# Kernel tuning notes

Measured on AMD Instinct MI355X. Metric: run time of the kernel, lower is better.

## Reference

```python
import jax, jax.numpy as jnp
import numpy as np

N = 100000
E = 1600000
IN, HID, OUT = 128, 256, 128


def setup_inputs() -> dict:
    key = jax.random.key(0)
    ks = jax.random.split(key, 8)
    x = jax.random.normal(ks[0], (N, IN), dtype=jnp.float32)
    edge_index = jax.random.randint(ks[1], (2, E), 0, N, dtype=jnp.int64)
    # PyG SAGEConv params: lin_l (neighbor aggr, with bias), lin_r (root, no bias)
    def glorot(k, shape):
        fan_in = shape[1]
        return jax.random.normal(k, shape, dtype=jnp.float32) / jnp.sqrt(jnp.float32(fan_in))
    W1l = glorot(ks[2], (HID, IN)); b1 = jnp.zeros((HID,), jnp.float32)
    W1r = glorot(ks[3], (HID, IN))
    W2l = glorot(ks[4], (OUT, HID)); b2 = jnp.zeros((OUT,), jnp.float32)
    W2r = glorot(ks[5], (OUT, HID))
    return {"x": x, "edge_index": edge_index, "W1l": W1l, "b1": b1,
            "W1r": W1r, "W2l": W2l, "b2": b2, "W2r": W2r}


def sage_conv(x, row, col, Wl, b, Wr, n_nodes):
    # mean-aggregate neighbor features x[row] at target nodes col
    msg = x[row]                                               # [E, d]
    s = jax.ops.segment_sum(msg, col, num_segments=n_nodes)    # [N, d]
    deg = jax.ops.segment_sum(jnp.ones((row.shape[0], 1), x.dtype), col,
                              num_segments=n_nodes)            # [N, 1]
    mean = s / jnp.maximum(deg, 1.0)
    return mean @ Wl.T + b + x @ Wr.T


def reference(x, edge_index, W1l, b1, W1r, W2l, b2, W2r):
    row, col = edge_index[0], edge_index[1]
    h = sage_conv(x, row, col, W1l, b1, W1r, N)
    h = jax.nn.relu(h)
    # dropout is identity in eval mode
    out = sage_conv(h, row, col, W2l, b2, W2r, N)
    return out
```

## Files before the change

kernel.cpp:

```cpp
#include <hip/hip_runtime.h>
#include <hip/hip_bf16.h>
#include <hip/hip_fp16.h>

#define NN 100000
#define NE 1600000
#define NCHUNK ((NN + 127) / 128)
#define NPB 512
#define NB 256
#define CHUNK 8192
#define NCH ((NE + CHUNK - 1) / CHUNK)

typedef __attribute__((ext_vector_type(8))) short short8;
typedef __attribute__((ext_vector_type(4))) float float4v;
typedef __attribute__((ext_vector_type(2))) float float2v;

__device__ __forceinline__ unsigned short f2bf(float f) {
    unsigned int b = __float_as_uint(f);
    return (unsigned short)((b + 0x7fffu + ((b >> 16) & 1u)) >> 16);
}
__device__ __forceinline__ unsigned int pack_bf16(float lo, float hi) {
    return (unsigned int)f2bf(lo) | ((unsigned int)f2bf(hi) << 16);
}
__device__ __forceinline__ void addp8(float* a, uint2 u) {
    float2v f;
    f = __builtin_amdgcn_cvt_pk_f32_fp8(u.x, false); a[0] += f.x; a[1] += f.y;
    f = __builtin_amdgcn_cvt_pk_f32_fp8(u.x, true);  a[2] += f.x; a[3] += f.y;
    f = __builtin_amdgcn_cvt_pk_f32_fp8(u.y, false); a[4] += f.x; a[5] += f.y;
    f = __builtin_amdgcn_cvt_pk_f32_fp8(u.y, true);  a[6] += f.x; a[7] += f.y;
}
__device__ __forceinline__ unsigned char f2fp8(float v) {
    int r = __builtin_amdgcn_cvt_pk_fp8_f32(v, v, 0, false);
    return (unsigned char)(r & 0xff);
}
__device__ __forceinline__ unsigned short pack2fp8(float lo, float hi) {
    int r = __builtin_amdgcn_cvt_pk_fp8_f32(lo, hi, 0, false);
    return (unsigned short)(r & 0xffff);
}
__device__ __forceinline__ float h2f(unsigned short u) {
    return __half2float(__ushort_as_half(u));
}

__global__ void k_prep(const float* x, const float* W1l, const float* W1r,
                       const float* W2l, const float* W2r, const int* ei,
                       unsigned int* axb_u, unsigned short* xf8, unsigned short* wb1,
                       unsigned short* wb2, int* bcnt) {
    __shared__ int hh[NB];
    int b = blockIdx.x, t = threadIdx.x;
    if (b < 25000) {
        int tt = b * 256 + t;
        int node = tt >> 6, i = tt & 63;
        float2 v = ((const float2*)x)[tt];
        axb_u[(size_t)node * 128 + 64 + i] = pack_bf16(v.x, v.y);
        xf8[(size_t)node * 64 + i] = pack2fp8(v.x, v.y);
    } else if (b < 25128) {
        int i = (b - 25000) * 256 + t;
        int r1 = i >> 7, c1 = i & 127;
        wb1[r1 * 256 + c1]       = f2bf(W1l[i]);
        wb1[r1 * 256 + 128 + c1] = f2bf(W1r[i]);
        wb2[i]         = f2bf(W2l[i]);
        wb2[32768 + i] = f2bf(W2r[i]);
    } else {
        hh[t] = 0;
        __syncthreads();
        int e0 = (b - 25128) * 6250;
        for (int e = e0 + t; e < e0 + 6250; e += 256)
            atomicAdd(&hh[ei[NE + e] >> 9], 1);
        __syncthreads();
        if (hh[t]) atomicAdd(&bcnt[t], hh[t]);
    }
}

__global__ void k_bscan(const int* bcnt, int* boff, int* bcur) {
    __shared__ int s[NB];
    int t = threadIdx.x;
    int v = bcnt[t];
    s[t] = v;
    __syncthreads();
    for (int d = 1; d < NB; d <<= 1) {
        int val = (t >= d) ? s[t - d] : 0;
        __syncthreads();
        s[t] += val;
        __syncthreads();
    }
    boff[t + 1] = s[t];
    if (t == 0) boff[0] = 0;
    bcur[t] = s[t] - v;
}

__global__ __launch_bounds__(256) void k_bscatter(const int* ei, int* bcur, unsigned int* pairs) {
    __shared__ unsigned int buf[CHUNK];
    __shared__ int cnt[NB];
    __shared__ int lbase[NB];
    __shared__ int lcur[NB];
    __shared__ int gpos[NB];
    int t = threadIdx.x;
    int e0 = blockIdx.x * CHUNK;
    int nedge = NE - e0; if (nedge > CHUNK) nedge = CHUNK;
    cnt[t] = 0;
    __syncthreads();
    for (int i = t; i < nedge; i += 256)
        atomicAdd(&cnt[ei[NE + e0 + i] >> 9], 1);
    __syncthreads();
    int v = cnt[t];
    lcur[t] = v;
    __syncthreads();
    for (int d = 1; d < NB; d <<= 1) {
        int val = (t >= d) ? lcur[t - d] : 0;
        __syncthreads();
        lcur[t] += val;
        __syncthreads();
    }
    lbase[t] = lcur[t] - v;
    gpos[t] = atomicAdd(&bcur[t], v);
    __syncthreads();
    lcur[t] = lbase[t];
    __syncthreads();
    for (int i = t; i < nedge; i += 256) {
        int r = ei[e0 + i], c = ei[NE + e0 + i];
        int b = c >> 9;
        int p = atomicAdd(&lcur[b], 1);
        buf[p] = (unsigned)r | ((unsigned)(c & 511) << 17);
    }
    __syncthreads();
    int wv = t >> 6, lane = t & 63;
    for (int b = wv; b < NB; b += 4) {
        int n = cnt[b], lb = lbase[b], gp = gpos[b];
        for (int i = lane; i < n; i += 64)
            pairs[gp + i] = buf[lb + i];
    }
}

__global__ __launch_bounds__(256) void k_build(const unsigned int* pairs, const int* boff,
                                               int* off, int* deg, int* csr) {
    __shared__ int ldeg[NPB];
    __shared__ int lcur[NPB];
    __shared__ int sscan[256];
    int b = blockIdx.x;
    int nbase = b * NPB;
    if (nbase >= NN) return;
    int t = threadIdx.x;
    int base = boff[b], cntb = boff[b + 1] - base;
    ldeg[t] = 0; ldeg[t + 256] = 0;
    __syncthreads();
    for (int i = t; i < cntb; i += 256) {
        unsigned int pr = pairs[base + i];
        atomicAdd(&ldeg[pr >> 17], 1);
    }
    __syncthreads();
    int d0 = ldeg[2 * t], d1 = ldeg[2 * t + 1];
    int v = d0 + d1;
    sscan[t] = v;
    __syncthreads();
    for (int d = 1; d < 256; d <<= 1) {
        int val = (t >= d) ? sscan[t - d] : 0;
        __syncthreads();
        sscan[t] += val;
        __syncthreads();
    }
    int ex = sscan[t] - v;
    lcur[2 * t] = ex; lcur[2 * t + 1] = ex + d0;
    __syncthreads();
    int nloc = NN - nbase; if (nloc > NPB) nloc = NPB;
    for (int ln = t; ln < nloc; ln += 256) {
        off[nbase + ln] = base + lcur[ln];
        deg[nbase + ln] = ldeg[ln];
    }
    __syncthreads();
    for (int i = t; i < cntb; i += 256) {
        unsigned int pr = pairs[base + i];
        int p = atomicAdd(&lcur[pr >> 17], 1);
        csr[base + p] = (int)(pr & 0x1FFFFu);
    }
}

__global__ void k_agg1(const uint2* xf8, const int* off, const int* deg,
                       const int* csr, unsigned int* axb_w) {
    int wid = (blockIdx.x * 256 + threadIdx.x) >> 6;
    if (wid >= NN) return;
    int lane = threadIdx.x & 63;
    int sub = lane >> 4, l16 = lane & 15;
    int start = off[wid], d = deg[wid];
    const uint2* gp = xf8 + l16;
    float a[8] = {0.f, 0.f, 0.f, 0.f, 0.f, 0.f, 0.f, 0.f};
    int j = sub;
    for (; j + 4 < d; j += 8) {
        int n0 = csr[start + j];
        int n1 = csr[start + j + 4];
        uint2 u0 = gp[(size_t)n0 * 16];
        uint2 u1 = gp[(size_t)n1 * 16];
        addp8(a, u0); addp8(a, u1);
    }
    if (j < d) {
        int nb = csr[start + j];
        uint2 u = gp[(size_t)nb * 16];
        addp8(a, u);
    }
#pragma unroll
    for (int i = 0; i < 8; i++) {
        a[i] += __shfl_xor(a[i], 16, 64);
        a[i] += __shfl_xor(a[i], 32, 64);
    }
    if (sub == 0) {
        float inv = 1.0f / (float)(d > 0 ? d : 1);
        uint4 o;
        o.x = pack_bf16(a[0] * inv, a[1] * inv);
        o.y = pack_bf16(a[2] * inv, a[3] * inv);
        o.z = pack_bf16(a[4] * inv, a[5] * inv);
        o.w = pack_bf16(a[6] * inv, a[7] * inv);
        *(uint4*)(axb_w + (size_t)wid * 128 + (l16 << 2)) = o;
    }
}

__global__ void k_agg2(const uint2* g, const int* off, const int* deg,
                       const int* csr, const unsigned short* partial, float* out) {
    int wid = (blockIdx.x * 256 + threadIdx.x) >> 6;
    if (wid >= NN) return;
    int lane = threadIdx.x & 63;
    int sub = lane >> 4, l16 = lane & 15;
    int start = off[wid], d = deg[wid];
    const uint2* gp = g + l16;
    float a[8] = {0.f, 0.f, 0.f, 0.f, 0.f, 0.f, 0.f, 0.f};
    int j = sub;
    for (; j + 4 < d; j += 8) {
        int n0 = csr[start + j];
        int n1 = csr[start + j + 4];
        uint2 u0 = gp[(size_t)n0 * 16];
        uint2 u1 = gp[(size_t)n1 * 16];
        addp8(a, u0); addp8(a, u1);
    }
    if (j < d) {
        int nb = csr[start + j];
        uint2 u = gp[(size_t)nb * 16];
        addp8(a, u);
    }
#pragma unroll
    for (int i = 0; i < 8; i++) {
        a[i] += __shfl_xor(a[i], 16, 64);
        a[i] += __shfl_xor(a[i], 32, 64);
    }
    if (sub == 0) {
        float inv = 1.0f / (float)(d > 0 ? d : 1);
        uint4 pu = *(const uint4*)(partial + (size_t)wid * 128 + (l16 << 3));
        float4 c0, c1;
        c0.x = h2f(pu.x & 0xffff) + a[0] * inv; c0.y = h2f(pu.x >> 16) + a[1] * inv;
        c0.z = h2f(pu.y & 0xffff) + a[2] * inv; c0.w = h2f(pu.y >> 16) + a[3] * inv;
        c1.x = h2f(pu.z & 0xffff) + a[4] * inv; c1.y = h2f(pu.z >> 16) + a[5] * inv;
        c1.z = h2f(pu.w & 0xffff) + a[6] * inv; c1.w = h2f(pu.w >> 16) + a[7] * inv;
        float4* po = (float4*)(out + (size_t)wid * 128) + (l16 << 1);
        po[0] = c0; po[1] = c1;
    }
}

#define BROW 264
__global__ __launch_bounds__(256, 4) void k_gemm1(const unsigned short* A, const unsigned short* wb,
                                                  const float* b1, unsigned short* H) {
    __shared__ unsigned short Bs[64 * BROW];
    int t = threadIdx.x;
    int cg = blockIdx.x & 3, chunk = blockIdx.x >> 2;
    {
        const short8* src = (const short8*)(wb + (size_t)cg * 64 * 256);
        short8* dst = (short8*)Bs;
#pragma unroll
        for (int i = 0; i < 8; i++) {
            int gi = i * 256 + t;
            int r = gi >> 5, c = gi & 31;
            dst[r * 33 + c] = src[gi];
        }
    }
    __syncthreads();
    int wv = t >> 6, lane = t & 63;
    int mrow = lane & 15, quad = lane >> 4;
    int base = chunk * 128 + wv * 32;
    if (base >= NN) return;
    float bias[4];
#pragma unroll
    for (int ctl = 0; ctl < 4; ctl++) bias[ctl] = b1[cg * 64 + ctl * 16 + mrow];
    float4v acc[2][4];
#pragma unroll
    for (int h = 0; h < 2; h++)
#pragma unroll
        for (int ctl = 0; ctl < 4; ctl++) acc[h][ctl] = (float4v)(0.0f);
    const short8* a0p = (const short8*)(A + (size_t)(base + mrow) * 256);
    const short8* a1p = (const short8*)(A + (size_t)(base + 16 + mrow) * 256);
#pragma unroll
    for (int kk = 0; kk < 8; kk++) {
        short8 a0 = a0p[kk * 4 + quad];
        short8 a1 = a1p[kk * 4 + quad];
        int koff = kk * 32 + quad * 8;
#pragma unroll
        for (int ctl = 0; ctl < 4; ctl++) {
            short8 b = *(const short8*)(Bs + (ctl * 16 + mrow) * BROW + koff);
            acc[0][ctl] = __builtin_amdgcn_mfma_f32_16x16x32_bf16(a0, b, acc[0][ctl], 0, 0, 0);
            acc[1][ctl] = __builtin_amdgcn_mfma_f32_16x16x32_bf16(a1, b, acc[1][ctl], 0, 0, 0);
        }
    }
#pragma unroll
    for (int ctl = 0; ctl < 4; ctl++) {
        int col = cg * 64 + ctl * 16 + mrow;
#pragma unroll
        for (int h = 0; h < 2; h++)
#pragma unroll
            for (int r = 0; r < 4; r++) {
                int node = base + h * 16 + quad * 4 + r;
                float v = acc[h][ctl][r] + bias[ctl];
                H[(size_t)node * 256 + col] = f2bf(fmaxf(v, 0.f));
            }
    }
}

__global__ __launch_bounds__(256, 4) void k_gemm2(const unsigned short* A, const unsigned short* wb,
                                                  const float* b2, unsigned char* g,
                                                  unsigned short* partial) {
    __shared__ unsigned short Bs[64 * BROW];
    int t = threadIdx.x;
    int cg = blockIdx.x & 3, chunk = blockIdx.x >> 2;
    {
        const short8* src = (const short8*)(wb + (size_t)cg * 64 * 256);
        short8* dst = (short8*)Bs;
#pragma unroll
        for (int i = 0; i < 8; i++) {
            int gi = i * 256 + t;
            int r = gi >> 5, c = gi & 31;
            dst[r * 33 + c] = src[gi];
        }
    }
    __syncthreads();
    int wv = t >> 6, lane = t & 63;
    int mrow = lane & 15, quad = lane >> 4;
    int base = chunk * 128 + wv * 32;
    if (base >= NN) return;
    float bias[4];
#pragma unroll
    for (int ctl = 0; ctl < 4; ctl++)
        bias[ctl] = (cg >= 2) ? b2[cg * 64 + ctl * 16 + mrow - 128] : 0.f;
    float4v acc[2][4];
#pragma unroll
    for (int h = 0; h < 2; h++)
#pragma unroll
        for (int ctl = 0; ctl < 4; ctl++) acc[h][ctl] = (float4v)(0.0f);
    const short8* a0p = (const short8*)(A + (size_t)(base + mrow) * 256);
    const short8* a1p = (const short8*)(A + (size_t)(base + 16 + mrow) * 256);
#pragma unroll
    for (int kk = 0; kk < 8; kk++) {
        short8 a0 = a0p[kk * 4 + quad];
        short8 a1 = a1p[kk * 4 + quad];
        int koff = kk * 32 + quad * 8;
#pragma unroll
        for (int ctl = 0; ctl < 4; ctl++) {
            short8 b = *(const short8*)(Bs + (ctl * 16 + mrow) * BROW + koff);
            acc[0][ctl] = __builtin_amdgcn_mfma_f32_16x16x32_bf16(a0, b, acc[0][ctl], 0, 0, 0);
            acc[1][ctl] = __builtin_amdgcn_mfma_f32_16x16x32_bf16(a1, b, acc[1][ctl], 0, 0, 0);
        }
    }
    if (cg < 2) {
#pragma unroll
        for (int ctl = 0; ctl < 4; ctl++) {
            int col = cg * 64 + ctl * 16 + mrow;
#pragma unroll
            for (int h = 0; h < 2; h++)
#pragma unroll
                for (int r = 0; r < 4; r++) {
                    int node = base + h * 16 + quad * 4 + r;
                    g[(size_t)node * 128 + col] = f2fp8(acc[h][ctl][r]);
                }
        }
    } else {
#pragma unroll
        for (int ctl = 0; ctl < 4; ctl++) {
            int pcol = cg * 64 + ctl * 16 + mrow - 128;
#pragma unroll
            for (int h = 0; h < 2; h++)
#pragma unroll
                for (int r = 0; r < 4; r++) {
                    int node = base + h * 16 + quad * 4 + r;
                    __half hf = __float2half(acc[h][ctl][r] + bias[ctl]);
                    partial[(size_t)node * 128 + pcol] = __half_as_ushort(hf);
                }
        }
    }
}

extern "C" void kernel_launch(void* const* d_in, const int* in_sizes, int n_in,
                              void* d_out, int out_size, void* d_ws, size_t ws_size,
                              hipStream_t stream) {
    const float* x   = (const float*)d_in[0];
    const int*   ei  = (const int*)d_in[1];
    const float* W1l = (const float*)d_in[2];
    const float* b1  = (const float*)d_in[3];
    const float* W1r = (const float*)d_in[4];
    const float* W2l = (const float*)d_in[5];
    const float* b2  = (const float*)d_in[6];
    const float* W2r = (const float*)d_in[7];
    float* out = (float*)d_out;

    char* p = (char*)d_ws;
    unsigned int* axb = (unsigned int*)p; p += (size_t)NN * 256 * 2;
    unsigned short* h = (unsigned short*)p; p += (size_t)NN * 256 * 2;
    unsigned char* g  = (unsigned char*)p; p += (size_t)NN * 128;
    unsigned short* xf8 = (unsigned short*)p; p += (size_t)NN * 128;
    unsigned short* wb1 = (unsigned short*)p; p += 65536 * 2;
    unsigned short* wb2 = (unsigned short*)p; p += 65536 * 2;
    int* deg  = (int*)p; p += (size_t)NN * 4;
    int* off  = (int*)p; p += (size_t)NN * 4;
    int* csr  = (int*)p; p += (size_t)NE * 4;
    int* bcnt = (int*)p; p += NB * 4;
    int* boff = (int*)p; p += (NB + 1) * 4;
    int* bcur = (int*)p; p += NB * 4;
    if (ws_size < (size_t)(p - (char*)d_ws)) return;
    unsigned int* pairs = (unsigned int*)h;
    unsigned short* partial = (unsigned short*)axb;

    hipMemsetAsync(bcnt, 0, NB * 4, stream);
    k_prep<<<25384, 256, 0, stream>>>(x, W1l, W1r, W2l, W2r, ei, axb, xf8, wb1, wb2, bcnt);
    k_bscan<<<1, NB, 0, stream>>>(bcnt, boff, bcur);
    k_bscatter<<<NCH, 256, 0, stream>>>(ei, bcur, pairs);
    k_build<<<NB, 256, 0, stream>>>(pairs, boff, off, deg, csr);
    k_agg1<<<NN * 64 / 256, 256, 0, stream>>>((const uint2*)xf8, off, deg, csr, axb);
    k_gemm1<<<NCHUNK * 4, 256, 0, stream>>>((const unsigned short*)axb, wb1, b1, h);
    k_gemm2<<<NCHUNK * 4, 256, 0, stream>>>(h, wb2, b2, g, partial);
    k_agg2<<<25000, 256, 0, stream>>>((const uint2*)g, off, deg, csr, partial, out);
}
```

Before: 373.3 us.

## Add padded 16-neighbor index table, grid-stride prep, swizzled GEMM grid, larger agg blocks

Builds a fixed-width table holding the first 16 neighbor indices of each node. The aggregation kernels load it with one coalesced read per lane and broadcast it with shuffles, avoiding serial CSR index loads for low-degree nodes. It also makes the prep kernel process 8 elements per thread with fewer blocks, reorders GEMM block indices so the 4 column groups of 8 chunks run together for better L2 reuse of A, uses 512-thread blocks in the aggregation kernels, and hoists the partial load in agg2 ahead of the gather loop. In exchange it adds extra workspace and writes in the CSR build, and the table is used only if the workspace is large enough.

```diff
diff --git a/kernel.cpp b/kernel.cpp
--- a/kernel.cpp
+++ b/kernel.cpp
@@ -46,14 +46,17 @@
                        unsigned short* wb2, int* bcnt) {
     __shared__ int hh[NB];
     int b = blockIdx.x, t = threadIdx.x;
-    if (b < 25000) {
-        int tt = b * 256 + t;
-        int node = tt >> 6, i = tt & 63;
-        float2 v = ((const float2*)x)[tt];
-        axb_u[(size_t)node * 128 + 64 + i] = pack_bf16(v.x, v.y);
-        xf8[(size_t)node * 64 + i] = pack2fp8(v.x, v.y);
-    } else if (b < 25128) {
-        int i = (b - 25000) * 256 + t;
+    if (b < 3125) {
+#pragma unroll
+        for (int k = 0; k < 8; k++) {
+            int tt = b * 2048 + k * 256 + t;
+            int node = tt >> 6, i = tt & 63;
+            float2 v = ((const float2*)x)[tt];
+            axb_u[(size_t)node * 128 + 64 + i] = pack_bf16(v.x, v.y);
+            xf8[(size_t)node * 64 + i] = pack2fp8(v.x, v.y);
+        }
+    } else if (b < 3253) {
+        int i = (b - 3125) * 256 + t;
         int r1 = i >> 7, c1 = i & 127;
         wb1[r1 * 256 + c1]       = f2bf(W1l[i]);
         wb1[r1 * 256 + 128 + c1] = f2bf(W1r[i]);
@@ -62,7 +65,7 @@
     } else {
         hh[t] = 0;
         __syncthreads();
-        int e0 = (b - 25128) * 6250;
+        int e0 = (b - 3253) * 6250;
         for (int e = e0 + t; e < e0 + 6250; e += 256)
             atomicAdd(&hh[ei[NE + e] >> 9], 1);
         __syncthreads();
@@ -131,9 +134,10 @@
 }
 
 __global__ __launch_bounds__(256) void k_build(const unsigned int* pairs, const int* boff,
-                                               int* off, int* deg, int* csr) {
+                                               int* off, int* deg, int* csr, int* csr16) {
     __shared__ int ldeg[NPB];
     __shared__ int lcur[NPB];
+    __shared__ int lini[NPB];
     __shared__ int sscan[256];
     int b = blockIdx.x;
     int nbase = b * NPB;
@@ -158,7 +162,8 @@
         __syncthreads();
     }
     int ex = sscan[t] - v;
-    lcur[2 * t] = ex; lcur[2 * t + 1] = ex + d0;
+    lcur[2 * t] = ex;      lcur[2 * t + 1] = ex + d0;
+    lini[2 * t] = ex;      lini[2 * t + 1] = ex + d0;
     __syncthreads();
     int nloc = NN - nbase; if (nloc > NPB) nloc = NPB;
     for (int ln = t; ln < nloc; ln += 256) {
@@ -166,23 +171,50 @@
         deg[nbase + ln] = ldeg[ln];
     }
     __syncthreads();
-    for (int i = t; i < cntb; i += 256) {
-        unsigned int pr = pairs[base + i];
-        int p = atomicAdd(&lcur[pr >> 17], 1);
-        csr[base + p] = (int)(pr & 0x1FFFFu);
-    }
-}
-
-__global__ void k_agg1(const uint2* xf8, const int* off, const int* deg,
-                       const int* csr, unsigned int* axb_w) {
-    int wid = (blockIdx.x * 256 + threadIdx.x) >> 6;
+    if (csr16) {
+        for (int i = t; i < cntb; i += 256) {
+            unsigned int pr = pairs[base + i];
+            int nd = pr >> 17;
+            int p = atomicAdd(&lcur[nd], 1);
+            int src = (int)(pr & 0x1FFFFu);
+            csr[base + p] = src;
+            int rk = p - lini[nd];
+            if (rk < 16) csr16[(size_t)(nbase + nd) * 16 + rk] = src;
+        }
+    } else {
+        for (int i = t; i < cntb; i += 256) {
+            unsigned int pr = pairs[base + i];
+            int p = atomicAdd(&lcur[pr >> 17], 1);
+            csr[base + p] = (int)(pr & 0x1FFFFu);
+        }
+    }
+}
+
+__global__ __launch_bounds__(512) void k_agg1(const uint2* xf8, const int* off, const int* deg,
+                                              const int* csr, const int* csr16,
+                                              unsigned int* axb_w) {
+    int wid = (blockIdx.x * 512 + threadIdx.x) >> 6;
     if (wid >= NN) return;
     int lane = threadIdx.x & 63;
     int sub = lane >> 4, l16 = lane & 15;
     int start = off[wid], d = deg[wid];
     const uint2* gp = xf8 + l16;
+    uint2 z; z.x = 0u; z.y = 0u;
     float a[8] = {0.f, 0.f, 0.f, 0.f, 0.f, 0.f, 0.f, 0.f};
-    int j = sub;
+    int j;
+    if (csr16) {
+        int e16 = csr16[(size_t)wid * 16 + l16];
+#pragma unroll
+        for (int r = 0; r < 4; r++) {
+            int rk = (r << 2) | sub;
+            int idx = __shfl(e16, rk, 64);
+            uint2 u = (rk < d) ? gp[(size_t)idx * 16] : z;
+            addp8(a, u);
+        }
+        j = 16 + sub;
+    } else {
+        j = sub;
+    }
     for (; j + 4 < d; j += 8) {
         int n0 = csr[start + j];
         int n1 = csr[start + j + 4];
@@ -211,16 +243,34 @@
     }
 }
 
-__global__ void k_agg2(const uint2* g, const int* off, const int* deg,
-                       const int* csr, const unsigned short* partial, float* out) {
-    int wid = (blockIdx.x * 256 + threadIdx.x) >> 6;
+__global__ __launch_bounds__(512) void k_agg2(const uint2* g, const int* off, const int* deg,
+                                              const int* csr, const int* csr16,
+                                              const unsigned short* partial, float* out) {
+    int wid = (blockIdx.x * 512 + threadIdx.x) >> 6;
     if (wid >= NN) return;
     int lane = threadIdx.x & 63;
     int sub = lane >> 4, l16 = lane & 15;
     int start = off[wid], d = deg[wid];
     const uint2* gp = g + l16;
+    uint2 z; z.x = 0u; z.y = 0u;
+    uint4 pu;
+    if (sub == 0)
+        pu = *(const uint4*)(partial + (size_t)wid * 128 + (l16 << 3));
     float a[8] = {0.f, 0.f, 0.f, 0.f, 0.f, 0.f, 0.f, 0.f};
-    int j = sub;
+    int j;
+    if (csr16) {
+        int e16 = csr16[(size_t)wid * 16 + l16];
+#pragma unroll
+        for (int r = 0; r < 4; r++) {
+            int rk = (r << 2) | sub;
+            int idx = __shfl(e16, rk, 64);
+            uint2 u = (rk < d) ? gp[(size_t)idx * 16] : z;
+            addp8(a, u);
+        }
+        j = 16 + sub;
+    } else {
+        j = sub;
+    }
     for (; j + 4 < d; j += 8) {
         int n0 = csr[start + j];
         int n1 = csr[start + j + 4];
@@ -240,7 +290,6 @@
     }
     if (sub == 0) {
         float inv = 1.0f / (float)(d > 0 ? d : 1);
-        uint4 pu = *(const uint4*)(partial + (size_t)wid * 128 + (l16 << 3));
         float4 c0, c1;
         c0.x = h2f(pu.x & 0xffff) + a[0] * inv; c0.y = h2f(pu.x >> 16) + a[1] * inv;
         c0.z = h2f(pu.y & 0xffff) + a[2] * inv; c0.w = h2f(pu.y >> 16) + a[3] * inv;
@@ -252,11 +301,15 @@
 }
 
 #define BROW 264
+#define GGRID (32 * ((NCHUNK + 7) / 8))
 __global__ __launch_bounds__(256, 4) void k_gemm1(const unsigned short* A, const unsigned short* wb,
                                                   const float* b1, unsigned short* H) {
     __shared__ unsigned short Bs[64 * BROW];
     int t = threadIdx.x;
-    int cg = blockIdx.x & 3, chunk = blockIdx.x >> 2;
+    int b = blockIdx.x;
+    int chunk = (b & 7) + ((b >> 5) << 3);
+    int cg = (b >> 3) & 3;
+    if (chunk >= NCHUNK) return;
     {
         const short8* src = (const short8*)(wb + (size_t)cg * 64 * 256);
         short8* dst = (short8*)Bs;
@@ -289,9 +342,9 @@
         int koff = kk * 32 + quad * 8;
 #pragma unroll
         for (int ctl = 0; ctl < 4; ctl++) {
-            short8 b = *(const short8*)(Bs + (ctl * 16 + mrow) * BROW + koff);
-            acc[0][ctl] = __builtin_amdgcn_mfma_f32_16x16x32_bf16(a0, b, acc[0][ctl], 0, 0, 0);
-            acc[1][ctl] = __builtin_amdgcn_mfma_f32_16x16x32_bf16(a1, b, acc[1][ctl], 0, 0, 0);
+            short8 bfr = *(const short8*)(Bs + (ctl * 16 + mrow) * BROW + koff);
+            acc[0][ctl] = __builtin_amdgcn_mfma_f32_16x16x32_bf16(a0, bfr, acc[0][ctl], 0, 0, 0);
+            acc[1][ctl] = __builtin_amdgcn_mfma_f32_16x16x32_bf16(a1, bfr, acc[1][ctl], 0, 0, 0);
         }
     }
 #pragma unroll
@@ -313,7 +366,10 @@
                                                   unsigned short* partial) {
     __shared__ unsigned short Bs[64 * BROW];
     int t = threadIdx.x;
-    int cg = blockIdx.x & 3, chunk = blockIdx.x >> 2;
+    int b = blockIdx.x;
+    int chunk = (b & 7) + ((b >> 5) << 3);
+    int cg = (b >> 3) & 3;
+    if (chunk >= NCHUNK) return;
     {
         const short8* src = (const short8*)(wb + (size_t)cg * 64 * 256);
         short8* dst = (short8*)Bs;
@@ -347,9 +403,9 @@
         int koff = kk * 32 + quad * 8;
 #pragma unroll
         for (int ctl = 0; ctl < 4; ctl++) {
-            short8 b = *(const short8*)(Bs + (ctl * 16 + mrow) * BROW + koff);
-            acc[0][ctl] = __builtin_amdgcn_mfma_f32_16x16x32_bf16(a0, b, acc[0][ctl], 0, 0, 0);
-            acc[1][ctl] = __builtin_amdgcn_mfma_f32_16x16x32_bf16(a1, b, acc[1][ctl], 0, 0, 0);
+            short8 bfr = *(const short8*)(Bs + (ctl * 16 + mrow) * BROW + koff);
+            acc[0][ctl] = __builtin_amdgcn_mfma_f32_16x16x32_bf16(a0, bfr, acc[0][ctl], 0, 0, 0);
+            acc[1][ctl] = __builtin_amdgcn_mfma_f32_16x16x32_bf16(a1, bfr, acc[1][ctl], 0, 0, 0);
         }
     }
     if (cg < 2) {
@@ -407,16 +463,18 @@
     int* boff = (int*)p; p += (NB + 1) * 4;
     int* bcur = (int*)p; p += NB * 4;
     if (ws_size < (size_t)(p - (char*)d_ws)) return;
+    int* csr16 = (int*)p; p += (size_t)NN * 16 * 4;
+    if (ws_size < (size_t)(p - (char*)d_ws)) csr16 = nullptr;
     unsigned int* pairs = (unsigned int*)h;
     unsigned short* partial = (unsigned short*)axb;
 
     hipMemsetAsync(bcnt, 0, NB * 4, stream);
-    k_prep<<<25384, 256, 0, stream>>>(x, W1l, W1r, W2l, W2r, ei, axb, xf8, wb1, wb2, bcnt);
+    k_prep<<<3509, 256, 0, stream>>>(x, W1l, W1r, W2l, W2r, ei, axb, xf8, wb1, wb2, bcnt);
     k_bscan<<<1, NB, 0, stream>>>(bcnt, boff, bcur);
     k_bscatter<<<NCH, 256, 0, stream>>>(ei, bcur, pairs);
-    k_build<<<NB, 256, 0, stream>>>(pairs, boff, off, deg, csr);
-    k_agg1<<<NN * 64 / 256, 256, 0, stream>>>((const uint2*)xf8, off, deg, csr, axb);
-    k_gemm1<<<NCHUNK * 4, 256, 0, stream>>>((const unsigned short*)axb, wb1, b1, h);
-    k_gemm2<<<NCHUNK * 4, 256, 0, stream>>>(h, wb2, b2, g, partial);
-    k_agg2<<<25000, 256, 0, stream>>>((const uint2*)g, off, deg, csr, partial, out);
-}
+    k_build<<<NB, 256, 0, stream>>>(pairs, boff, off, deg, csr, csr16);
+    k_agg1<<<12500, 512, 0, stream>>>((const uint2*)xf8, off, deg, csr, csr16, axb);
+    k_gemm1<<<GGRID, 256, 0, stream>>>((const unsigned short*)axb, wb1, b1, h);
+    k_gemm2<<<GGRID, 256, 0, stream>>>(h, wb2, b2, g, partial);
+    k_agg2<<<12500, 512, 0, stream>>>((const uint2*)g, off, deg, csr, csr16, partial, out);
+}
```

Result: faster. 356.1 us (-4.6%).
